# Kernel optimization log

Measured on AMD Instinct MI355X. Metric: run time of the kernel, lower is better.

The kernel has to match this reference:

```python
import jax, jax.numpy as jnp
import numpy as np
import math

D_MODEL = 512
KEY_DIM = 128
NUM_LAYERS = 2
TEMP = 30.0
NORM_EPS = 1e-5
NORM_SCALE = math.sqrt(1.0 / (D_MODEL * 4 * 4))


def _l2norm_lastdim(x):
    # F.normalize(x, p=2, dim=-1): x / max(||x||, 1e-12)
    n = jnp.sqrt(jnp.sum(x * x, axis=-1, keepdims=True))
    return x / jnp.maximum(n, 1e-12)


def _attn(q, k, v, WK, bK):
    # q: [Sq,B,D], k: [Sk,B,D], v: [Sk,B,D] -> [Sq,B,D]
    wq = _l2norm_lastdim(q @ WK + bK)            # [Sq,B,K]
    wk = _l2norm_lastdim(k @ WK + bK)            # [Sk,B,K]
    dot = jnp.einsum('qbk,sbk->bqs', wq, wk)     # cosine sims
    aff = jax.nn.softmax(dot * TEMP, axis=-1)
    return jnp.einsum('bqs,sbd->qbd', aff, v)


def _instance_norm(x, h, w):
    # x: [HW,B,D]; InstanceL2Norm over (D,h,w) per batch element, size_average=True
    HW, B, D = x.shape
    ss = jnp.sum(x * x, axis=(0, 2))             # [B]
    factor = NORM_SCALE * jnp.sqrt((D * h * w) / (ss + NORM_EPS))
    return x * factor[None, :, None]


def _encoder(src4d, WKs, bKs):
    B, D, H, W = src4d.shape
    x = src4d.reshape(B, D, H * W).transpose(2, 0, 1)   # [HW,B,D]
    for _ in range(NUM_LAYERS):
        x = _instance_norm(x + _attn(x, x, x, WKs, bKs), H, W)
    return x  # memory [HW,B,D]


def _decoder(tgt4d, memory, pos, WKs, bKs, WKc, bKc):
    B, D, H, W = tgt4d.shape
    x = tgt4d.reshape(B, D, H * W).transpose(2, 0, 1)   # [HW,B,D]
    for _ in range(NUM_LAYERS):
        x = _instance_norm(x + _attn(x, x, x, WKs, bKs), H, W)
        mask = _attn(x, memory, pos, WKc, bKc)
        t2 = _instance_norm(x * mask, H, W)
        t3 = _attn(x, memory, memory * pos, WKc, bKc)
        t4 = _instance_norm(x + t3, H, W)
        x = _instance_norm(t2 + t4, H, W)
    feat = x.reshape(H, W, B, D).transpose(2, 3, 0, 1)  # [B,D,H,W]
    return feat


def setup_inputs() -> dict:
    key = jax.random.key(0)
    k1, k2, k3, k4, k5 = jax.random.split(key, 5)
    B, D, H, W = 16, D_MODEL, 32, 32
    std = math.sqrt(2.0 / KEY_DIM)
    return {
        'train_feat': jax.random.normal(k1, (B, D, H, W), jnp.float32),
        'test_feat': jax.random.normal(k2, (B, D, H, W), jnp.float32),
        'train_label': jax.random.uniform(k3, (B, H, W), jnp.float32),
        'WK_self': jax.random.normal(k4, (D, KEY_DIM), jnp.float32) * std,
        'bK_self': jnp.zeros((KEY_DIM,), jnp.float32),
        'WK_cross': jax.random.normal(k5, (D, KEY_DIM), jnp.float32) * std,
        'bK_cross': jnp.zeros((KEY_DIM,), jnp.float32),
    }


def reference(train_feat, test_feat, train_label, WK_self, bK_self, WK_cross, bK_cross):
    B, D, H, W = train_feat.shape
    memory = _encoder(train_feat, WK_self, bK_self)              # [HW,B,D]
    # pos: label [B,H,W] -> [HW,B,1] -> broadcast to [HW,B,D]
    pos = jnp.broadcast_to(train_label.reshape(B, H * W).T[:, :, None], (H * W, B, D))
    encoded_feat = _decoder(train_feat, memory, pos, WK_self, bK_self, WK_cross, bK_cross)
    decoded_feat = _decoder(test_feat, memory, pos, WK_self, bK_self, WK_cross, bK_cross)
    return (encoded_feat, decoded_feat)
```

## Files before the change

kernel.cpp:

```cpp
#include <hip/hip_runtime.h>
#include <math.h>

#define NB 16
#define SEQ 1024
#define DM 512
#define KD 128
#define TEMP_F 30.0f
#define NS_F 0.011048543456039805f
#define DS_F 524288.0f

#define SS_IDX(grp, b) (((grp) * NB + (b)) * 16)
#define SS_STRIDE 768
#define SS_STAGES 12
#define SS_FLOATS (SS_STRIDE * SS_STAGES)

#define PSTR 72

typedef short bf16x8 __attribute__((ext_vector_type(8)));
typedef float f32x4 __attribute__((ext_vector_type(4)));
typedef unsigned short us;
typedef unsigned short us4v __attribute__((ext_vector_type(4)));
typedef unsigned short us8 __attribute__((ext_vector_type(8)));

__device__ __forceinline__ us f2bf(float x) {
    union { float f; unsigned u; } v; v.f = x;
    unsigned r = v.u + 0x7fffu + ((v.u >> 16) & 1u);
    return (us)(r >> 16);
}
__device__ __forceinline__ float bf2f(us h) {
    union { unsigned u; float f; } v; v.u = ((unsigned)h) << 16;
    return v.f;
}

#define GLL16(gp, lp) __builtin_amdgcn_global_load_lds( \
    (__attribute__((address_space(1))) void*)(unsigned long long)(gp), \
    (__attribute__((address_space(3))) void*)(unsigned)(unsigned long long)(lp), 16, 0, 0)

__global__ __launch_bounds__(256) void k_transpose_in(const float* __restrict__ src,
                                                      us* __restrict__ XC,
                                                      us* __restrict__ XT) {
    __shared__ float tile[32][33];
    const int b = blockIdx.z;
    const int d0 = blockIdx.x * 32;
    const int s0 = blockIdx.y * 32;
    const int tx = threadIdx.x, ty = threadIdx.y;
    const float* p = src + (size_t)b * DM * SEQ;
    us* pt = XT + (size_t)b * DM * SEQ;
    us* pc = XC + (size_t)b * SEQ * 1024;
#pragma unroll
    for (int j = 0; j < 32; j += 8) {
        const size_t o = (size_t)(d0 + ty + j) * SEQ + s0 + tx;
        const float v = p[o];
        tile[ty + j][tx] = v;
        pt[o] = f2bf(v);
    }
    __syncthreads();
#pragma unroll
    for (int j = 0; j < 4; ++j) {
        const int s = s0 + ty + j * 8;
        const int d = d0 + tx;
        const float v = tile[tx][ty + j * 8];
        const us h = f2bf(v);
        pc[(size_t)s * 1024 + d] = h;
        pc[(size_t)s * 1024 + 512 + d] = f2bf(v - bf2f(h));
    }
}

__global__ __launch_bounds__(256) void k_mklabel(const us* __restrict__ MT,
                                                 const float* __restrict__ label,
                                                 us* __restrict__ ML) {
    const int b = blockIdx.y;
    const size_t off = ((size_t)blockIdx.x * 256 + threadIdx.x) * 8;
    const int s = (int)(off & (SEQ - 1));
    const size_t o = (size_t)b * DM * SEQ + off;
    us8 v = *(const us8*)(MT + o);
    const float4 l0 = *(const float4*)(label + (size_t)b * SEQ + s);
    const float4 l1 = *(const float4*)(label + (size_t)b * SEQ + s + 4);
    us8 r;
    r[0] = f2bf(bf2f(v[0]) * l0.x); r[1] = f2bf(bf2f(v[1]) * l0.y);
    r[2] = f2bf(bf2f(v[2]) * l0.z); r[3] = f2bf(bf2f(v[3]) * l0.w);
    r[4] = f2bf(bf2f(v[4]) * l1.x); r[5] = f2bf(bf2f(v[5]) * l1.y);
    r[6] = f2bf(bf2f(v[6]) * l1.z); r[7] = f2bf(bf2f(v[7]) * l1.w);
    *(us8*)(ML + o) = r;
}

__global__ __launch_bounds__(256) void k_wsplit(const float* __restrict__ WK,
                                                us* __restrict__ WC) {
    const int k = blockIdx.x;
    for (int d = threadIdx.x; d < DM; d += 256) {
        const float v = WK[(size_t)d * KD + k];
        const us h = f2bf(v);
        WC[(size_t)k * 1024 + d] = h;
        WC[(size_t)k * 1024 + 512 + d] = f2bf(v - bf2f(h));
    }
}

__global__ __launch_bounds__(256) void k_proj(const us* __restrict__ XC,
                                              const us* __restrict__ WC,
                                              const float* __restrict__ bK,
                                              us* __restrict__ Wout) {
    const int row0 = blockIdx.x * 32;
    __shared__ short As[32 * 64], Bs[128 * 64];
    __shared__ float ssp[2][32];
    const int tid = threadIdx.x, w = tid >> 6, l = tid & 63;
    const int wm = (w >> 1) * 16, wn = (w & 1) * 64;
    const int sr = l >> 3, sc = (((l & 7) ^ (l >> 3)) << 3);
    const int lr = l & 15, lk = (l >> 4) * 8;
    const int sx = (lr & 7) << 3;
    f32x4 acc[4] = {};
    for (int k0 = 0; k0 < 1536; k0 += 64) {
        const int ak0 = (k0 < 1024) ? k0 : k0 - 1024;
        const int bk0 = (k0 < 512) ? k0 : k0 - 512;
        GLL16(XC + (size_t)(row0 + w * 8 + sr) * 1024 + ak0 + sc, &As[w * 512]);
#pragma unroll
        for (int cc = 0; cc < 4; ++cc) {
            const int c = 4 * w + cc;
            GLL16(WC + (size_t)(c * 8 + sr) * 1024 + bk0 + sc, &Bs[c * 512]);
        }
        __syncthreads();
#pragma unroll
        for (int kc = 0; kc < 2; ++kc) {
            const int kk = kc * 32 + lk;
            const bf16x8 a = *(const bf16x8*)&As[(wm + lr) * 64 + (kk ^ sx)];
            bf16x8 bb[4];
#pragma unroll
            for (int fn = 0; fn < 4; ++fn)
                bb[fn] = *(const bf16x8*)&Bs[(wn + fn * 16 + lr) * 64 + (kk ^ sx)];
#pragma unroll
            for (int fn = 0; fn < 4; ++fn)
                acc[fn] = __builtin_amdgcn_mfma_f32_16x16x32_bf16(a, bb[fn], acc[fn], 0, 0, 0);
        }
        __syncthreads();
    }
    const int er = l & 15, eq = (l >> 4) * 4;
    const int nh = w & 1;
    float bkv[4];
#pragma unroll
    for (int fn = 0; fn < 4; ++fn) bkv[fn] = bK[wn + fn * 16 + er];
    float vv[4][4];
#pragma unroll
    for (int r = 0; r < 4; ++r) {
        float ss = 0.f;
#pragma unroll
        for (int fn = 0; fn < 4; ++fn) {
            const float t = acc[fn][r] + bkv[fn];
            vv[fn][r] = t;
            ss += t * t;
        }
#pragma unroll
        for (int o = 8; o > 0; o >>= 1) ss += __shfl_xor(ss, o, 64);
        if (er == 0) ssp[nh][wm + eq + r] = ss;
    }
    __syncthreads();
#pragma unroll
    for (int r = 0; r < 4; ++r) {
        const int rowloc = wm + eq + r;
        const float tot = ssp[0][rowloc] + ssp[1][rowloc];
        const float invn = 1.0f / fmaxf(sqrtf(tot), 1e-12f);
        const size_t ro = (size_t)(row0 + rowloc) * 256;
#pragma unroll
        for (int fn = 0; fn < 4; ++fn) {
            const float ov = vv[fn][r] * invn;
            const us h = f2bf(ov);
            Wout[ro + wn + fn * 16 + er] = h;
            Wout[ro + 128 + wn + fn * 16 + er] = f2bf(ov - bf2f(h));
        }
    }
}

__global__ __launch_bounds__(512, 2) void k_attn(const us* __restrict__ Qc,
                                                 const us* __restrict__ Kc,
                                                 const us* __restrict__ VT,
                                                 const us* __restrict__ XC,
                                                 const float* __restrict__ labelp,
                                                 float* __restrict__ MVEC,
                                                 float* __restrict__ Cout,
                                                 float* __restrict__ SS, int mode) {
    const int b = blockIdx.x;
    const int q0 = blockIdx.y * 64;
    __shared__ short KL[2][4 * 64 * 64];
    __shared__ us PL[64 * PSTR];
    __shared__ float RSL[2][64], RLL[2][64];
    __shared__ float INVL[64], MVL[64];
    __shared__ float ps[3][8];
    const int tid = threadIdx.x, w = tid >> 6, l = tid & 63;
    const int lr = l & 15, g = l >> 4, lk = g * 8;
    const int qa = w & 3, sh = w >> 2;
    const int kx = (lr & 7) << 3;
    const us* Qb = Qc + (size_t)b * SEQ * 256;
    const us* Kb = Kc + (size_t)b * SEQ * 256;
    const us* Vb = VT + (size_t)b * DM * SEQ;
    const float* Lb = labelp ? labelp + (size_t)b * SEQ : nullptr;

    const us* Qrow = Qb + (size_t)(q0 + qa * 16 + lr) * 256;
    bf16x8 qh[4], ql[4];
#pragma unroll
    for (int kc = 0; kc < 4; ++kc) {
        qh[kc] = *(const bf16x8*)(Qrow + kc * 32 + lk);
        ql[kc] = *(const bf16x8*)(Qrow + 128 + kc * 32 + lk);
    }
#pragma unroll
    for (int i = 0; i < 4; ++i) {
        const int c = w * 4 + i, p = c & 3, rg = c >> 2;
        GLL16(Kb + (size_t)(rg * 8 + (l >> 3)) * 256 + p * 64 + (((l & 7) ^ (l >> 3)) << 3),
              &KL[0][p * 4096 + rg * 512 + l * 8]);
    }
    __syncthreads();

    f32x4 acc[4][4];
#pragma unroll
    for (int m = 0; m < 4; ++m)
#pragma unroll
        for (int n = 0; n < 4; ++n) acc[m][n] = (f32x4){0.f, 0.f, 0.f, 0.f};
    float rs = 0.f, rl = 0.f;
    int cur = 0;
    for (int it = 0; it < 16; ++it) {
        const int s0 = it * 64;
        bf16x8 vb0[4];
#pragma unroll
        for (int n = 0; n < 4; ++n)
            vb0[n] = *(const bf16x8*)(Vb + (size_t)(w * 64 + n * 16 + lr) * 1024 + s0 + lk);
#pragma unroll
        for (int sn = 0; sn < 2; ++sn) {
            const int srow = sh * 32 + sn * 16 + lr;
            const int rowb = srow * 64;
            f32x4 sacc = {};
            bf16x8 kf[4];
#pragma unroll
            for (int kc = 0; kc < 4; ++kc)
                kf[kc] = *(const bf16x8*)&KL[cur][(kc >> 1) * 4096 + rowb + ((((kc & 1) << 5) + lk) ^ kx)];
            __builtin_amdgcn_s_setprio(1);
#pragma unroll
            for (int kc = 0; kc < 4; ++kc)
                sacc = __builtin_amdgcn_mfma_f32_16x16x32_bf16(kf[kc], qh[kc], sacc, 0, 0, 0);
#pragma unroll
            for (int kc = 0; kc < 4; ++kc)
                sacc = __builtin_amdgcn_mfma_f32_16x16x32_bf16(kf[kc], ql[kc], sacc, 0, 0, 0);
            __builtin_amdgcn_s_setprio(0);
#pragma unroll
            for (int kc = 0; kc < 4; ++kc)
                kf[kc] = *(const bf16x8*)&KL[cur][(2 + (kc >> 1)) * 4096 + rowb + ((((kc & 1) << 5) + lk) ^ kx)];
            __builtin_amdgcn_s_setprio(1);
#pragma unroll
            for (int kc = 0; kc < 4; ++kc)
                sacc = __builtin_amdgcn_mfma_f32_16x16x32_bf16(kf[kc], qh[kc], sacc, 0, 0, 0);
            __builtin_amdgcn_s_setprio(0);
            const int sbase = sh * 32 + sn * 16 + g * 4;
            float lb4[4] = {0.f, 0.f, 0.f, 0.f};
            if (mode == 2) {
                const float4 t = *(const float4*)(Lb + s0 + sbase);
                lb4[0] = t.x; lb4[1] = t.y; lb4[2] = t.z; lb4[3] = t.w;
            }
            us4v pw;
#pragma unroll
            for (int r = 0; r < 4; ++r) {
                const float e = __expf(fmaf(TEMP_F, sacc[r], -TEMP_F));
                rs += e;
                rl += e * lb4[r];
                pw[r] = f2bf(e);
            }
            *(us4v*)&PL[(qa * 16 + lr) * PSTR + sbase] = pw;
        }
        __syncthreads();
        bf16x8 vb1[4];
#pragma unroll
        for (int n = 0; n < 4; ++n)
            vb1[n] = *(const bf16x8*)(Vb + (size_t)(w * 64 + n * 16 + lr) * 1024 + s0 + 32 + lk);
        if (it < 15) {
            const int s1 = s0 + 64, nb2 = cur ^ 1;
#pragma unroll
            for (int i = 0; i < 4; ++i) {
                const int c = w * 4 + i, p = c & 3, rg = c >> 2;
                GLL16(Kb + (size_t)(s1 + rg * 8 + (l >> 3)) * 256 + p * 64 + (((l & 7) ^ (l >> 3)) << 3),
                      &KL[nb2][p * 4096 + rg * 512 + l * 8]);
            }
        }
        bf16x8 pa[4];
#pragma unroll
        for (int m = 0; m < 4; ++m)
            pa[m] = *(const bf16x8*)&PL[(m * 16 + lr) * PSTR + lk];
        __builtin_amdgcn_s_setprio(1);
#pragma unroll
        for (int m = 0; m < 4; ++m)
#pragma unroll
            for (int n = 0; n < 4; ++n)
                acc[m][n] = __builtin_amdgcn_mfma_f32_16x16x32_bf16(pa[m], vb0[n], acc[m][n], 0, 0, 0);
        __builtin_amdgcn_s_setprio(0);
#pragma unroll
        for (int m = 0; m < 4; ++m)
            pa[m] = *(const bf16x8*)&PL[(m * 16 + lr) * PSTR + 32 + lk];
        __builtin_amdgcn_s_setprio(1);
#pragma unroll
        for (int m = 0; m < 4; ++m)
#pragma unroll
            for (int n = 0; n < 4; ++n)
                acc[m][n] = __builtin_amdgcn_mfma_f32_16x16x32_bf16(pa[m], vb1[n], acc[m][n], 0, 0, 0);
        __builtin_amdgcn_s_setprio(0);
        __syncthreads();
        cur ^= 1;
    }

    rs += __shfl_xor(rs, 16, 64);
    rs += __shfl_xor(rs, 32, 64);
    rl += __shfl_xor(rl, 16, 64);
    rl += __shfl_xor(rl, 32, 64);
    if (g == 0) {
        RSL[sh][qa * 16 + lr] = rs;
        RLL[sh][qa * 16 + lr] = rl;
    }
    __syncthreads();
    if (tid < 64) {
        const float tot = RSL[0][tid] + RSL[1][tid];
        const float iv = 1.0f / tot;
        INVL[tid] = iv;
        const float mvv = (RLL[0][tid] + RLL[1][tid]) * iv;
        MVL[tid] = mvv;
        if (mode == 2) MVEC[(size_t)b * SEQ + q0 + tid] = mvv;
    }
    __syncthreads();

    const us* XCb = XC + (size_t)b * SEQ * 1024;
    float sa = 0.f, sb = 0.f, sab = 0.f;
#pragma unroll
    for (int m = 0; m < 4; ++m)
#pragma unroll
        for (int r = 0; r < 4; ++r) {
            const int q = m * 16 + g * 4 + r;
            const float iv = INVL[q];
            const float mvq = MVL[q];
            const int row = q0 + q;
#pragma unroll
            for (int n = 0; n < 4; ++n) {
                const int col = w * 64 + n * 16 + lr;
                float v = acc[m][n][r] * iv;
                const size_t o = ((size_t)b * SEQ + row) * DM + col;
                const size_t xo = (size_t)row * 1024 + col;
                const float x = bf2f(XCb[xo]) + bf2f(XCb[xo + 512]);
                v += x;
                sb += v * v;
                if (mode == 2) { const float a = x * mvq; sa += a * a; sab += a * v; }
                Cout[o] = v;
            }
        }
#pragma unroll
    for (int off = 32; off > 0; off >>= 1) {
        sb += __shfl_xor(sb, off, 64);
        if (mode == 2) { sa += __shfl_xor(sa, off, 64); sab += __shfl_xor(sab, off, 64); }
    }
    if (l == 0) { ps[0][w] = sb; ps[1][w] = sa; ps[2][w] = sab; }
    __syncthreads();
    if (tid == 0) {
        float t0 = 0.f, t1 = 0.f, t2 = 0.f;
#pragma unroll
        for (int i = 0; i < 8; ++i) { t0 += ps[0][i]; t1 += ps[1][i]; t2 += ps[2][i]; }
        if (mode == 1) {
            atomicAdd(&SS[SS_IDX(0, b)], t0);
        } else {
            atomicAdd(&SS[SS_IDX(0, b)], t1);
            atomicAdd(&SS[SS_IDX(1, b)], t0);
            atomicAdd(&SS[SS_IDX(2, b)], t2);
        }
    }
}

__global__ void k_zero(float* __restrict__ SSb) {
    const int i = blockIdx.x * 256 + threadIdx.x;
    if (i < SS_FLOATS) SSb[i] = 0.0f;
}

__global__ __launch_bounds__(256) void k_finish(const float* __restrict__ Tin,
                                                const us* __restrict__ XCin,
                                                const float* __restrict__ mv,
                                                const float* __restrict__ SS,
                                                us* __restrict__ XCout,
                                                us* __restrict__ XTb,
                                                float* __restrict__ XTf,
                                                int mode, int writeXC) {
    const int b = blockIdx.z;
    const int s0 = blockIdx.x * 32, d0 = blockIdx.y * 32;
    const int tx = threadIdx.x, ty = threadIdx.y;
    __shared__ float tile[32][33];
    float f1 = 0.f, f2 = 0.f, f3;
    if (mode == 0) {
        f3 = NS_F * sqrtf(DS_F / (SS[SS_IDX(0, b)] + 1e-5f));
    } else {
        const float ssa = SS[SS_IDX(0, b)], ssb = SS[SS_IDX(1, b)], ssab = SS[SS_IDX(2, b)];
        f1 = NS_F * sqrtf(DS_F / (ssa + 1e-5f));
        f2 = NS_F * sqrtf(DS_F / (ssb + 1e-5f));
        const float ssc = f1 * f1 * ssa + 2.f * f1 * f2 * ssab + f2 * f2 * ssb;
        f3 = NS_F * sqrtf(DS_F / (ssc + 1e-5f));
    }
#pragma unroll
    for (int j = 0; j < 4; ++j) {
        const int s = s0 + ty + j * 8;
        const int d = d0 + tx;
        const size_t o = ((size_t)b * SEQ + s) * DM + d;
        const size_t xo = ((size_t)b * SEQ + s) * 1024 + d;
        float v;
        if (mode == 0) v = f3 * Tin[o];
        else {
            const float x = bf2f(XCin[xo]) + bf2f(XCin[xo + 512]);
            v = f3 * (f1 * x * mv[(size_t)b * SEQ + s] + f2 * Tin[o]);
        }
        if (writeXC) {
            const us h = f2bf(v);
            XCout[xo] = h;
            XCout[xo + 512] = f2bf(v - bf2f(h));
        }
        tile[ty + j * 8][tx] = v;
    }
    __syncthreads();
#pragma unroll
    for (int j = 0; j < 4; ++j) {
        const int d = d0 + ty + j * 8;
        const int s = s0 + tx;
        const float v = tile[tx][ty + j * 8];
        const size_t o = ((size_t)b * DM + d) * SEQ + s;
        if (XTb) XTb[o] = f2bf(v);
        else if (XTf) XTf[o] = v;
    }
}

extern "C" void kernel_launch(void* const* d_in, const int* in_sizes, int n_in,
                              void* d_out, int out_size, void* d_ws, size_t ws_size,
                              hipStream_t stream) {
    const float* train_feat = (const float*)d_in[0];
    const float* test_feat  = (const float*)d_in[1];
    const float* label      = (const float*)d_in[2];
    const float* WKs        = (const float*)d_in[3];
    const float* bKs        = (const float*)d_in[4];
    const float* WKc        = (const float*)d_in[5];
    const float* bKc        = (const float*)d_in[6];
    float* out = (float*)d_out;
    float* w = (float*)d_ws;

    const size_t SBD = (size_t)NB * SEQ * DM;
    const size_t SBK = (size_t)NB * SEQ * KD;

    float* T   = w;
    us* XC     = (us*)(T + SBD);
    us* XTd    = XC + 2 * SBD;
    us* MEMT   = XTd + SBD;
    us* MEMLT  = MEMT + SBD;
    us* W1C    = MEMLT + SBD;
    us* WKMC   = W1C + 2 * SBK;
    us* WCs    = WKMC + 2 * SBK;
    us* WCc    = WCs + (size_t)KD * 1024;
    float* MVEC = (float*)(WCc + (size_t)KD * 1024);
    float* SS   = MVEC + (size_t)NB * SEQ;

    const dim3 gT_in(DM / 32, SEQ / 32, NB), bT(32, 8);
    const dim3 gFin(SEQ / 32, DM / 32, NB);
    const dim3 gAtt(NB, SEQ / 64);

    int stage = 0;
    auto nextSS = [&]() { return SS + (size_t)(stage++) * SS_STRIDE; };

    k_zero<<<(SS_FLOATS + 255) / 256, 256, 0, stream>>>(SS);
    k_wsplit<<<KD, 256, 0, stream>>>(WKs, WCs);
    k_wsplit<<<KD, 256, 0, stream>>>(WKc, WCc);

    k_transpose_in<<<gT_in, bT, 0, stream>>>(train_feat, XC, MEMT);
    for (int l = 0; l < 2; ++l) {
        float* SSst = nextSS();
        k_proj<<<NB * SEQ / 32, 256, 0, stream>>>(XC, WCs, bKs, W1C);
        k_attn<<<gAtt, 512, 0, stream>>>(W1C, W1C, MEMT, XC, nullptr, nullptr, T, SSst, 1);
        k_finish<<<gFin, bT, 0, stream>>>(T, XC, nullptr, SSst, XC, MEMT, nullptr, 0, 1);
    }
    k_proj<<<NB * SEQ / 32, 256, 0, stream>>>(XC, WCc, bKc, WKMC);
    k_mklabel<<<dim3(DM * SEQ / 8 / 256, NB), 256, 0, stream>>>(MEMT, label, MEMLT);

    auto decoder = [&](const float* feat, float* outp) {
        k_transpose_in<<<gT_in, bT, 0, stream>>>(feat, XC, XTd);
        for (int l = 0; l < 2; ++l) {
            float* SSst = nextSS();
            k_proj<<<NB * SEQ / 32, 256, 0, stream>>>(XC, WCs, bKs, W1C);
            k_attn<<<gAtt, 512, 0, stream>>>(W1C, W1C, XTd, XC, nullptr, nullptr, T, SSst, 1);
            k_finish<<<gFin, bT, 0, stream>>>(T, XC, nullptr, SSst, XC, XTd, nullptr, 0, 1);
            float* SSst2 = nextSS();
            k_proj<<<NB * SEQ / 32, 256, 0, stream>>>(XC, WCc, bKc, W1C);
            k_attn<<<gAtt, 512, 0, stream>>>(W1C, WKMC, MEMLT, XC, label, MVEC, T, SSst2, 2);
            if (l == 0)
                k_finish<<<gFin, bT, 0, stream>>>(T, XC, MVEC, SSst2, XC, XTd, nullptr, 1, 1);
            else
                k_finish<<<gFin, bT, 0, stream>>>(T, XC, MVEC, SSst2, XC, nullptr, outp, 1, 0);
        }
    };
    decoder(train_feat, out);
    decoder(test_feat, out + SBD);
}
```

Before: 1.007 ms.

## Batch both decoders into a single 32-batch pass sharing encoder memory

The train and test decoders now run together as one 32-element batch when the workspace is large enough, so every projection, attention and finish kernel launches once with twice the grid instead of twice sequentially. The attention kernel takes a kv mask so that cross-attention blocks index the shared 16-batch memory and label, while self-attention uses its own batch. This is meant to halve the launch count for the decoder phase and fill the GPU better with larger grids. It costs a larger workspace layout and a fallback path, and it relies on the SS index scheme growing to 32 batches.

```diff
diff --git a/kernel.cpp b/kernel.cpp
--- a/kernel.cpp
+++ b/kernel.cpp
@@ -9,8 +9,8 @@
 #define NS_F 0.011048543456039805f
 #define DS_F 524288.0f
 
-#define SS_IDX(grp, b) (((grp) * NB + (b)) * 16)
-#define SS_STRIDE 768
+#define SS_IDX(grp, b) (((grp) * 32 + (b)) * 16)
+#define SS_STRIDE 1536
 #define SS_STAGES 12
 #define SS_FLOATS (SS_STRIDE * SS_STAGES)
 
@@ -175,8 +175,9 @@
                                                  const float* __restrict__ labelp,
                                                  float* __restrict__ MVEC,
                                                  float* __restrict__ Cout,
-                                                 float* __restrict__ SS, int mode) {
+                                                 float* __restrict__ SS, int mode, int kvmask) {
     const int b = blockIdx.x;
+    const int bkv = b & kvmask;
     const int q0 = blockIdx.y * 64;
     __shared__ short KL[2][4 * 64 * 64];
     __shared__ us PL[64 * PSTR];
@@ -188,9 +189,9 @@
     const int qa = w & 3, sh = w >> 2;
     const int kx = (lr & 7) << 3;
     const us* Qb = Qc + (size_t)b * SEQ * 256;
-    const us* Kb = Kc + (size_t)b * SEQ * 256;
-    const us* Vb = VT + (size_t)b * DM * SEQ;
-    const float* Lb = labelp ? labelp + (size_t)b * SEQ : nullptr;
+    const us* Kb = Kc + (size_t)bkv * SEQ * 256;
+    const us* Vb = VT + (size_t)bkv * DM * SEQ;
+    const float* Lb = labelp ? labelp + (size_t)(bkv & 15) * SEQ : nullptr;
 
     const us* Qrow = Qb + (size_t)(q0 + qa * 16 + lr) * 256;
     bf16x8 qh[4], ql[4];
@@ -434,24 +435,30 @@
     float* out = (float*)d_out;
     float* w = (float*)d_ws;
 
-    const size_t SBD = (size_t)NB * SEQ * DM;
-    const size_t SBK = (size_t)NB * SEQ * KD;
-
-    float* T   = w;
-    us* XC     = (us*)(T + SBD);
-    us* XTd    = XC + 2 * SBD;
-    us* MEMT   = XTd + SBD;
-    us* MEMLT  = MEMT + SBD;
-    us* W1C    = MEMLT + SBD;
-    us* WKMC   = W1C + 2 * SBK;
-    us* WCs    = WKMC + 2 * SBK;
-    us* WCc    = WCs + (size_t)KD * 1024;
+    const size_t PB  = (size_t)SEQ * DM;
+    const size_t SBD = (size_t)NB * PB;
+
+    auto needF = [&](size_t nbat) {
+        return nbat * (PB  + PB  + PB / 2  + PB / 4  + 1024 )
+             + (size_t)NB * (PB / 2  + PB / 2  + PB / 4 )
+             + 2 * (size_t)KD * 512  + SS_FLOATS + 4096;
+    };
+    const size_t wsf = ws_size / 4;
+    const int nbat = (wsf >= needF(32)) ? 32 : NB;
+
+    float* T    = w;
+    us* XC      = (us*)(T + (size_t)nbat * PB);
+    us* XTd     = XC + (size_t)nbat * 2 * PB;
+    us* W1C     = XTd + (size_t)nbat * PB;
+    us* MEMT    = W1C + (size_t)nbat * PB / 2;
+    us* MEMLT   = MEMT + (size_t)NB * PB;
+    us* WKMC    = MEMLT + (size_t)NB * PB;
+    us* WCs     = WKMC + (size_t)NB * PB / 2;
+    us* WCc     = WCs + (size_t)KD * 1024;
     float* MVEC = (float*)(WCc + (size_t)KD * 1024);
-    float* SS   = MVEC + (size_t)NB * SEQ;
+    float* SS   = MVEC + (size_t)nbat * SEQ;
 
     const dim3 gT_in(DM / 32, SEQ / 32, NB), bT(32, 8);
-    const dim3 gFin(SEQ / 32, DM / 32, NB);
-    const dim3 gAtt(NB, SEQ / 64);
 
     int stage = 0;
     auto nextSS = [&]() { return SS + (size_t)(stage++) * SS_STRIDE; };
@@ -464,28 +471,38 @@
     for (int l = 0; l < 2; ++l) {
         float* SSst = nextSS();
         k_proj<<<NB * SEQ / 32, 256, 0, stream>>>(XC, WCs, bKs, W1C);
-        k_attn<<<gAtt, 512, 0, stream>>>(W1C, W1C, MEMT, XC, nullptr, nullptr, T, SSst, 1);
-        k_finish<<<gFin, bT, 0, stream>>>(T, XC, nullptr, SSst, XC, MEMT, nullptr, 0, 1);
+        k_attn<<<dim3(NB, SEQ / 64), 512, 0, stream>>>(W1C, W1C, MEMT, XC, nullptr, nullptr, T, SSst, 1, 63);
+        k_finish<<<dim3(SEQ / 32, DM / 32, NB), bT, 0, stream>>>(T, XC, nullptr, SSst, XC, MEMT, nullptr, 0, 1);
     }
     k_proj<<<NB * SEQ / 32, 256, 0, stream>>>(XC, WCc, bKc, WKMC);
     k_mklabel<<<dim3(DM * SEQ / 8 / 256, NB), 256, 0, stream>>>(MEMT, label, MEMLT);
 
-    auto decoder = [&](const float* feat, float* outp) {
-        k_transpose_in<<<gT_in, bT, 0, stream>>>(feat, XC, XTd);
+    auto dec_layers = [&](int db, float* outp) {
+        const dim3 gA(db, SEQ / 64);
+        const dim3 gF(SEQ / 32, DM / 32, db);
         for (int l = 0; l < 2; ++l) {
             float* SSst = nextSS();
-            k_proj<<<NB * SEQ / 32, 256, 0, stream>>>(XC, WCs, bKs, W1C);
-            k_attn<<<gAtt, 512, 0, stream>>>(W1C, W1C, XTd, XC, nullptr, nullptr, T, SSst, 1);
-            k_finish<<<gFin, bT, 0, stream>>>(T, XC, nullptr, SSst, XC, XTd, nullptr, 0, 1);
+            k_proj<<<db * SEQ / 32, 256, 0, stream>>>(XC, WCs, bKs, W1C);
+            k_attn<<<gA, 512, 0, stream>>>(W1C, W1C, XTd, XC, nullptr, nullptr, T, SSst, 1, 63);
+            k_finish<<<gF, bT, 0, stream>>>(T, XC, nullptr, SSst, XC, XTd, nullptr, 0, 1);
             float* SSst2 = nextSS();
-            k_proj<<<NB * SEQ / 32, 256, 0, stream>>>(XC, WCc, bKc, W1C);
-            k_attn<<<gAtt, 512, 0, stream>>>(W1C, WKMC, MEMLT, XC, label, MVEC, T, SSst2, 2);
+            k_proj<<<db * SEQ / 32, 256, 0, stream>>>(XC, WCc, bKc, W1C);
+            k_attn<<<gA, 512, 0, stream>>>(W1C, WKMC, MEMLT, XC, label, MVEC, T, SSst2, 2, 15);
             if (l == 0)
-                k_finish<<<gFin, bT, 0, stream>>>(T, XC, MVEC, SSst2, XC, XTd, nullptr, 1, 1);
+                k_finish<<<gF, bT, 0, stream>>>(T, XC, MVEC, SSst2, XC, XTd, nullptr, 1, 1);
             else
-                k_finish<<<gFin, bT, 0, stream>>>(T, XC, MVEC, SSst2, XC, nullptr, outp, 1, 0);
+                k_finish<<<gF, bT, 0, stream>>>(T, XC, MVEC, SSst2, XC, nullptr, outp, 1, 0);
         }
     };
-    decoder(train_feat, out);
-    decoder(test_feat, out + SBD);
-}
+
+    if (nbat == 32) {
+        k_transpose_in<<<gT_in, bT, 0, stream>>>(train_feat, XC, XTd);
+        k_transpose_in<<<gT_in, bT, 0, stream>>>(test_feat, XC + (size_t)NB * 2 * PB, XTd + (size_t)NB * PB);
+        dec_layers(32, out);
+    } else {
+        k_transpose_in<<<gT_in, bT, 0, stream>>>(train_feat, XC, XTd);
+        dec_layers(NB, out);
+        k_transpose_in<<<gT_in, bT, 0, stream>>>(test_feat, XC, XTd);
+        dec_layers(NB, out + SBD);
+    }
+}
```

Measured after the change: 959.4 us. -4.7%, faster.
